# Performance work log

Hardware: AMD Instinct MI355X
Metric: run time of the kernel (lower is better)

## Reference

```python
import jax, jax.numpy as jnp
import numpy as np

NUM_QRYS = 300
NUM_CLASSES = 80
NUM_PAIRS = 4_000_000
NMS_CANDIDATES = 1000
NMS_THR = 0.65
MAX_SEGS = 100
REFINED_WEIGHT = 2.0
FH = FW = 256  # final mask grid resolution


def setup_inputs() -> dict:
    key = jax.random.key(0)
    k1, k2, k3, k4, k5, k6, k7 = jax.random.split(key, 7)
    cls_logits = jax.random.normal(k1, (NUM_QRYS, NUM_CLASSES + 1), jnp.float32)
    # valid xyxy boxes in normalized [0,1] coords
    b = jax.random.uniform(k2, (NUM_QRYS, 4), jnp.float32)
    x1 = b[:, 0] * 0.7
    y1 = b[:, 1] * 0.7
    x2 = x1 + 0.05 + b[:, 2] * 0.25
    y2 = y1 + 0.05 + b[:, 3] * 0.25
    pred_boxes = jnp.stack([x1, y1, x2, y2], axis=1)
    seg_logits = jax.random.normal(k3, (NUM_PAIRS,), jnp.float32)
    key_xy = jax.random.uniform(k4, (NUM_PAIRS, 2), jnp.float32)
    qry_ids = jax.random.randint(k5, (NUM_PAIRS,), 0, NUM_QRYS, jnp.int32)
    refined_mask = jax.random.randint(k6, (NUM_PAIRS,), 0, 2, jnp.int32).astype(bool)
    map_ids = jax.random.randint(k7, (NUM_PAIRS,), 0, 4, jnp.int32)
    return {"cls_logits": cls_logits, "pred_boxes": pred_boxes, "seg_logits": seg_logits,
            "key_xy": key_xy, "qry_ids": qry_ids, "refined_mask": refined_mask, "map_ids": map_ids}


def _box_iou(boxes):  # boxes: [C,4] xyxy -> [C,C]
    x1 = jnp.maximum(boxes[:, None, 0], boxes[None, :, 0])
    y1 = jnp.maximum(boxes[:, None, 1], boxes[None, :, 1])
    x2 = jnp.minimum(boxes[:, None, 2], boxes[None, :, 2])
    y2 = jnp.minimum(boxes[:, None, 3], boxes[None, :, 3])
    inter = jnp.clip(x2 - x1, 0.0) * jnp.clip(y2 - y1, 0.0)
    area = (boxes[:, 2] - boxes[:, 0]) * (boxes[:, 3] - boxes[:, 1])
    union = area[:, None] + area[None, :] - inter
    return inter / jnp.maximum(union, 1e-9)


def _nms_keep(iou, thr):
    # greedy NMS over score-sorted candidates (rows already in descending score order)
    C = iou.shape[0]
    idx = jnp.arange(C)
    def body(i, keep):
        sup = (iou[i] > thr) & (idx > i) & keep[i]
        return keep & ~sup
    return jax.lax.fori_loop(0, C, body, jnp.ones(C, dtype=bool))


def reference(cls_logits, pred_boxes, seg_logits, key_xy, qry_ids, refined_mask, map_ids):
    num_qrys = cls_logits.shape[0]
    # expand per-query class scores -> flat predictions (batch_size = 1)
    scores = jax.nn.sigmoid(cls_logits[:, :-1]).reshape(-1)          # [Q*C]
    feat_ids = jnp.repeat(jnp.arange(num_qrys), NUM_CLASSES)          # [Q*C]
    labels = jnp.tile(jnp.arange(NUM_CLASSES), num_qrys)              # [Q*C]
    # top-k candidates before NMS
    top_scores, cand = jax.lax.top_k(scores, NMS_CANDIDATES)
    cand_feats = feat_ids[cand]
    cand_labels = labels[cand]
    # class-aware (batched) NMS: offset boxes per label so classes don't suppress each other
    offs = cand_labels.astype(pred_boxes.dtype)[:, None] * 4.0
    cand_boxes = pred_boxes[cand_feats] + offs
    keep = _nms_keep(_box_iou(cand_boxes), NMS_THR)
    kept_scores = jnp.where(keep, top_scores, -jnp.inf)
    sel_scores, sel = jax.lax.top_k(kept_scores, MAX_SEGS)
    sel_scores = jnp.where(jnp.isfinite(sel_scores), sel_scores, 0.0)
    sel_feats = cand_feats[sel]
    # assemble per-query mask logit maps from sparse query-key pairs (scatter-max)
    px = jnp.clip((key_xy[:, 0] * FW).astype(jnp.int32), 0, FW - 1)
    py = jnp.clip((key_xy[:, 1] * FH).astype(jnp.int32), 0, FH - 1)
    w_logits = jnp.where(refined_mask, REFINED_WEIGHT * seg_logits, seg_logits)
    flat = qry_ids * (FH * FW) + py * FW + px                          # [num_pairs]
    qry_maps = jnp.full((num_qrys * FH * FW,), -1e4, cls_logits.dtype).at[flat].max(w_logits)
    qry_maps = qry_maps.reshape(num_qrys, FH, FW)
    mask_probs = jax.nn.sigmoid(qry_maps[sel_feats])                   # [MAX_SEGS, FH, FW]
    # score-weighted soft masks (float output; thresholding at mask_thr yields bool masks)
    return sel_scores[:, None, None] * mask_probs
```

## Files before the change

kernel.cpp:

```cpp
#include <hip/hip_runtime.h>

#define NQ        300
#define NC        80
#define NE        24000
#define CAND      1000
#define KSEL      100
#define NPAIRS    4000000
#define HB        4096
#define FHW       65536
#define NMS_THR_F 0.65f
#define MAPS_INIT 0x39E3BFFFu

#define NBLK_A    977
#define SLOT_CAP  32768

__device__ __forceinline__ unsigned enc_f32(float f) {
    unsigned u = __float_as_uint(f);
    return (u & 0x80000000u) ? ~u : (u | 0x80000000u);
}
__device__ __forceinline__ float dec_f32(unsigned k) {
    unsigned u = (k & 0x80000000u) ? (k ^ 0x80000000u) : ~k;
    return __uint_as_float(u);
}

__global__ __launch_bounds__(1024) void k_select(
    const float* __restrict__ cls,
    const float* __restrict__ pboxes,
    float4* __restrict__ cboxes, float* __restrict__ cscore,
    int* __restrict__ cfeat, int* __restrict__ clabel,
    unsigned* __restrict__ slot_tail)
{
    __shared__ unsigned long long sbuf[4096];
    unsigned* hist = (unsigned*)sbuf;
    __shared__ unsigned subhist[64];
    __shared__ int sB, sT, sAbove, sCount, sN;
    int tid = threadIdx.x;

    if (tid < KSEL) slot_tail[tid] = 0u;

    for (int b = tid; b < HB; b += 1024) hist[b] = 0u;
    if (tid < 64) subhist[tid] = 0u;
    __syncthreads();

    unsigned long long lk[24];
    #pragma unroll
    for (int k = 0; k < 24; k++) {
        int e = tid + (k << 10);
        if (e < NE) {
            int q = e / NC, c = e - q * NC;
            float x = cls[q * (NC + 1) + c];
            float s = 1.f / (1.f + expf(-x));
            unsigned bits = __float_as_uint(s);
            lk[k] = ((unsigned long long)bits << 32) | (unsigned)(0xFFFFFFFFu - (unsigned)e);
            atomicAdd(&hist[bits >> 18], 1u);
        }
    }
    __syncthreads();

    if (tid == 0) {
        int acc = 0, B = 0;
        for (int b = HB - 1; b >= 0; b--) {
            acc += (int)hist[b];
            if (acc >= CAND) { B = b; break; }
        }
        sB = B; sAbove = acc - (int)hist[B]; sCount = 0;
    }
    __syncthreads();
    unsigned B = (unsigned)sB;

    #pragma unroll
    for (int k = 0; k < 24; k++) {
        int e = tid + (k << 10);
        if (e < NE && (unsigned)(lk[k] >> 50) == B)
            atomicAdd(&subhist[(unsigned)(lk[k] >> 44) & 63u], 1u);
    }
    __syncthreads();
    if (tid == 0) {
        int acc2 = sAbove, T = 0;
        for (int t = 63; t >= 0; t--) {
            acc2 += (int)subhist[t];
            if (acc2 >= CAND) { T = t; break; }
        }
        sT = T; sN = acc2;
    }
    __syncthreads();
    unsigned T = (unsigned)sT;

    #pragma unroll
    for (int k = 0; k < 24; k++) {
        int e = tid + (k << 10);
        if (e < NE) {
            unsigned long long key = lk[k];
            unsigned bkt = (unsigned)(key >> 50);
            unsigned sub = (unsigned)(key >> 44) & 63u;
            if (bkt > B || (bkt == B && sub >= T)) {
                int pos = atomicAdd(&sCount, 1);
                if (pos < 4096) sbuf[pos] = key;
            }
        }
    }
    __syncthreads();
    int n = min(sN, 4096);

    if (n <= 1024) {
        unsigned long long r = (tid < n) ? sbuf[tid] : 0ULL;
        for (int k = 2; k <= 1024; k <<= 1) {
            for (int j = k >> 1; j > 0; j >>= 1) {
                unsigned long long p;
                if (j >= 64) {
                    sbuf[tid] = r; __syncthreads();
                    p = sbuf[tid ^ j]; __syncthreads();
                } else {
                    p = __shfl_xor(r, j, 64);
                }
                bool d = (tid & k) != 0, lower = (tid & j) == 0;
                r = (d != lower) ? (r > p ? r : p) : (r < p ? r : p);
            }
        }
        sbuf[tid] = r;
        __syncthreads();
    } else {
        int nsort = 2048; while (nsort < n) nsort <<= 1;
        for (int i = n + tid; i < nsort; i += 1024) sbuf[i] = 0ULL;
        __syncthreads();
        for (int k = 2; k <= nsort; k <<= 1) {
            for (int j = k >> 1; j > 0; j >>= 1) {
                for (int i = tid; i < nsort; i += 1024) {
                    int ixj = i ^ j;
                    if (ixj > i) {
                        unsigned long long a = sbuf[i], b = sbuf[ixj];
                        bool up = ((i & k) == 0);
                        if (up ? (a < b) : (a > b)) { sbuf[i] = b; sbuf[ixj] = a; }
                    }
                }
                __syncthreads();
            }
        }
    }

    if (tid < CAND) {
        unsigned long long key = sbuf[tid];
        unsigned bits = (unsigned)(key >> 32);
        unsigned e = 0xFFFFFFFFu - (unsigned)(key & 0xFFFFFFFFu);
        int feat = (int)e / NC, lab = (int)e - feat * NC;
        cscore[tid] = __uint_as_float(bits);
        cfeat[tid]  = feat;
        clabel[tid] = lab;
        float off = 4.f * (float)lab;
        float4 b;
        b.x = pboxes[feat * 4 + 0] + off; b.y = pboxes[feat * 4 + 1] + off;
        b.z = pboxes[feat * 4 + 2] + off; b.w = pboxes[feat * 4 + 3] + off;
        cboxes[tid] = b;
    }
}

__global__ __launch_bounds__(64) void k_nms(
    const float4* __restrict__ cboxes, const int* __restrict__ clabel,
    int* __restrict__ keepflag)
{
    int lab = blockIdx.x, lane = threadIdx.x;
    __shared__ int list[256];
    int base = 0;
    for (int c = 0; c < CAND; c += 64) {
        int i = c + lane;
        bool m = (i < CAND) && (clabel[i] == lab);
        unsigned long long bal = __ballot(m);
        int rank = __popcll(bal & ((1ULL << lane) - 1ULL));
        if (m && base + rank < 256) list[base + rank] = i;
        base += __popcll(bal);
    }
    __syncthreads();
    int n = min(base, 256);

    float4 bx[4]; float area[4];
    unsigned keepm = 0;
    #pragma unroll
    for (int s = 0; s < 4; s++) {
        int j = (s << 6) + lane;
        if (j < n) {
            bx[s] = cboxes[list[j]];
            area[s] = (bx[s].z - bx[s].x) * (bx[s].w - bx[s].y);
            keepm |= (1u << s);
        }
    }
    #pragma unroll
    for (int slot = 0; slot < 4; slot++) {
        int i0 = slot << 6;
        if (i0 >= n) break;
        int iend = min(64, n - i0);
        for (int l = 0; l < iend; l++) {
            int i = i0 + l;
            unsigned km = __shfl(keepm, l);
            bool keep_i = (km >> slot) & 1u;
            float bix = __shfl(bx[slot].x, l), biy = __shfl(bx[slot].y, l);
            float biz = __shfl(bx[slot].z, l), biw = __shfl(bx[slot].w, l);
            float ai  = __shfl(area[slot], l);
            if (keep_i) {
                #pragma unroll
                for (int s2 = 0; s2 < 4; s2++) {
                    int j = (s2 << 6) + lane;
                    if (j > i && j < n && ((keepm >> s2) & 1u)) {
                        float xx1 = fmaxf(bix, bx[s2].x), yy1 = fmaxf(biy, bx[s2].y);
                        float xx2 = fminf(biz, bx[s2].z), yy2 = fminf(biw, bx[s2].w);
                        float inter = fmaxf(xx2 - xx1, 0.f) * fmaxf(yy2 - yy1, 0.f);
                        float uni = ai + area[s2] - inter;
                        if (inter / fmaxf(uni, 1e-9f) > NMS_THR_F) keepm &= ~(1u << s2);
                    }
                }
            }
        }
    }
    #pragma unroll
    for (int s = 0; s < 4; s++) {
        int j = (s << 6) + lane;
        if (j < n) keepflag[list[j]] = (keepm >> s) & 1u;
    }
}

__global__ __launch_bounds__(64) void k_pick(
    const float* __restrict__ cscore, const int* __restrict__ cfeat,
    const int* __restrict__ keepflag,
    float* __restrict__ sel_score, int* __restrict__ sel_slot,
    int* __restrict__ qry2slot,
    const unsigned* __restrict__ refined_raw, unsigned* __restrict__ mode_flag)
{
    int lane = threadIdx.x;
    __shared__ float ss[KSEL];
    __shared__ int   sf[KSEL];
    __shared__ int   q2s[NQ];

    unsigned any = 0;
    for (int i = lane; i < 4096; i += 64) if (refined_raw[i] > 1u) any = 1;
    unsigned mode = (__ballot(any != 0) != 0ULL) ? 1u : 0u;

    int base = 0;
    for (int c = 0; c < CAND; c += 64) {
        int i = c + lane;
        bool k = (i < CAND) && (keepflag[i] != 0);
        unsigned long long bal = __ballot(k);
        int rank = __popcll(bal & ((1ULL << lane) - 1ULL));
        int pos = base + rank;
        if (k && pos < KSEL) { ss[pos] = cscore[i]; sf[pos] = cfeat[i]; }
        base += __popcll(bal);
    }
    for (int q = lane; q < NQ; q += 64) q2s[q] = -1;
    __syncthreads();
    if (lane == 0) {
        int nsel = min(base, KSEL), nslots = 0;
        for (int s = 0; s < KSEL; s++) {
            if (s < nsel) {
                int f = sf[s];
                int sl = q2s[f];
                if (sl < 0) { sl = nslots++; q2s[f] = sl; }
                sel_slot[s] = sl; sel_score[s] = ss[s];
            } else {
                sel_slot[s] = -1; sel_score[s] = 0.f;
            }
        }
        *mode_flag = mode;
    }
    __syncthreads();
    for (int q = lane; q < NQ; q += 64) qry2slot[q] = q2s[q];
}

__global__ __launch_bounds__(1024) void k_stage(
    const float4* __restrict__ seg4, const float4* __restrict__ xy4,
    const int4* __restrict__ qry4, const unsigned* __restrict__ refined_raw,
    const int* __restrict__ qry2slot, const unsigned* __restrict__ mode_flag,
    unsigned long long* __restrict__ bins, unsigned* __restrict__ slot_tail)
{
    __shared__ unsigned hist[KSEL];
    __shared__ unsigned gbase[KSEL];
    int tid = threadIdx.x, b = blockIdx.x;
    if (tid < KSEL) hist[tid] = 0u;
    __syncthreads();

    int t = b * 1024 + tid;
    unsigned addr[4], encw[4], rnk[4]; int nloc = 0;
    if (t < (NPAIRS / 4)) {
        int4 q = qry4[t];
        int s0 = qry2slot[q.x], s1 = qry2slot[q.y];
        int s2 = qry2slot[q.z], s3 = qry2slot[q.w];
        if ((s0 & s1 & s2 & s3) >= 0 || s0 >= 0 || s1 >= 0 || s2 >= 0 || s3 >= 0) {
            float4 sg   = seg4[t];
            float4 xy01 = xy4[2 * t], xy23 = xy4[2 * t + 1];
            unsigned r0, r1, r2, r3;
            if (*mode_flag) {
                unsigned rb = refined_raw[t];
                r0 = rb & 255u; r1 = (rb >> 8) & 255u; r2 = (rb >> 16) & 255u; r3 = rb >> 24;
            } else {
                uint4 rr = ((const uint4*)refined_raw)[t];
                r0 = rr.x; r1 = rr.y; r2 = rr.z; r3 = rr.w;
            }
            #define MK_REC(S, PX, PY, W, R)                                       \
                if (S >= 0) {                                                     \
                    int px = min(max((int)((PX) * 256.f), 0), 255);               \
                    int py = min(max((int)((PY) * 256.f), 0), 255);               \
                    float w = (R) ? 2.f * (W) : (W);                              \
                    addr[nloc] = ((unsigned)S << 16) | ((unsigned)py << 8) | (unsigned)px; \
                    encw[nloc] = enc_f32(w);                                      \
                    rnk[nloc]  = atomicAdd(&hist[S], 1u);                         \
                    nloc++;                                                       \
                }
            MK_REC(s0, xy01.x, xy01.y, sg.x, r0)
            MK_REC(s1, xy01.z, xy01.w, sg.y, r1)
            MK_REC(s2, xy23.x, xy23.y, sg.z, r2)
            MK_REC(s3, xy23.z, xy23.w, sg.w, r3)
            #undef MK_REC
        }
    }
    __syncthreads();
    if (tid < KSEL && hist[tid] > 0u)
        gbase[tid] = atomicAdd(&slot_tail[tid], hist[tid]);
    __syncthreads();

    for (int k = 0; k < nloc; k++) {
        unsigned s = addr[k] >> 16;
        unsigned pos = gbase[s] + rnk[k];
        if (pos < SLOT_CAP)
            bins[(size_t)s * SLOT_CAP + pos] =
                ((unsigned long long)encw[k] << 32) | addr[k];
    }
}

__global__ __launch_bounds__(1024) void k_tile_out(
    const unsigned long long* __restrict__ bins,
    const unsigned* __restrict__ slot_tail,
    const float* __restrict__ sel_score, const int* __restrict__ sel_slot,
    float4* __restrict__ out4)
{
    __shared__ unsigned tile[8192];
    int tid = threadIdx.x;
    int i = blockIdx.x >> 3, h = blockIdx.x & 7;
    int slot = sel_slot[i];
    float sc = sel_score[i];
    long obase = (long)i * (FHW / 4) + h * 2048;

    if (slot < 0) {
        float4 z = {0.f, 0.f, 0.f, 0.f};
        out4[obase + tid] = z;
        out4[obase + 1024 + tid] = z;
        return;
    }

    #pragma unroll
    for (int k = 0; k < 8; k++) tile[tid + (k << 10)] = MAPS_INIT;
    __syncthreads();

    unsigned tot = min(slot_tail[slot], (unsigned)SLOT_CAP);
    const unsigned long long* seg = bins + (size_t)slot * SLOT_CAP;
    for (unsigned j = tid; j < tot; j += 1024) {
        unsigned long long r = seg[j];
        unsigned addr = (unsigned)r;
        if (((addr >> 13) & 7u) == (unsigned)h)
            atomicMax(&tile[addr & 8191u], (unsigned)(r >> 32));
    }
    __syncthreads();

    #pragma unroll
    for (int k = 0; k < 2; k++) {
        int j = tid + (k << 10);
        unsigned m0 = tile[4 * j + 0], m1 = tile[4 * j + 1];
        unsigned m2 = tile[4 * j + 2], m3 = tile[4 * j + 3];
        float4 v;
        v.x = sc / (1.f + expf(-dec_f32(m0)));
        v.y = sc / (1.f + expf(-dec_f32(m1)));
        v.z = sc / (1.f + expf(-dec_f32(m2)));
        v.w = sc / (1.f + expf(-dec_f32(m3)));
        out4[obase + j] = v;
    }
}

extern "C" void kernel_launch(void* const* d_in, const int* in_sizes, int n_in,
                              void* d_out, int out_size, void* d_ws, size_t ws_size,
                              hipStream_t stream) {
    const float*    cls     = (const float*)d_in[0];
    const float*    pboxes  = (const float*)d_in[1];
    const float4*   seg4    = (const float4*)d_in[2];
    const float4*   xy4     = (const float4*)d_in[3];
    const int4*     qry4    = (const int4*)d_in[4];
    const unsigned* refined = (const unsigned*)d_in[5];
    float* out = (float*)d_out;

    char* ws = (char*)d_ws;
    unsigned long long* bins = (unsigned long long*)ws;
    unsigned*  slot_tail = (unsigned*)(ws + 26214400);
    float4*    cboxes    = (float4*)  (ws + 26214800);
    float*     cscore    = (float*)   (ws + 26230800);
    int*       cfeat     = (int*)     (ws + 26234800);
    int*       clabel    = (int*)     (ws + 26238800);
    int*       keepflag  = (int*)     (ws + 26242800);
    float*     sel_score = (float*)   (ws + 26246800);
    int*       sel_slot  = (int*)     (ws + 26247200);
    int*       qry2slot  = (int*)     (ws + 26247600);
    unsigned*  mode_flag = (unsigned*)(ws + 26248800);

    k_select  <<<1, 1024, 0, stream>>>(cls, pboxes, cboxes, cscore, cfeat, clabel,
                                       slot_tail);
    k_nms     <<<NC, 64, 0, stream>>>(cboxes, clabel, keepflag);
    k_pick    <<<1, 64, 0, stream>>>(cscore, cfeat, keepflag, sel_score, sel_slot,
                                     qry2slot, refined, mode_flag);
    k_stage   <<<NBLK_A, 1024, 0, stream>>>(seg4, xy4, qry4, refined, qry2slot, mode_flag,
                                            bins, slot_tail);
    k_tile_out<<<KSEL * 8, 1024, 0, stream>>>(bins, slot_tail, sel_score, sel_slot,
                                              (float4*)out);
}
```

Before: 242.5 us.

## Fuse all five stages into one cooperative persistent kernel with grid syncs

Replaces the five separate launches (select, NMS, pick, stage, tile output) with a single cooperative kernel of 256 blocks that separates phases with grid.sync(). Score computation and histogramming now run across the whole grid into global scratch, while selection stays in block 0. Staging and tiling loop over persistent blocks. The goal is to remove per-launch overhead and the idle gaps between small serial kernels. In exchange it pays grid-wide barrier costs, leaves most blocks idle during the single-block phases, and runs the bandwidth-heavy phases with fewer blocks.

```diff
diff --git a/kernel.cpp b/kernel.cpp
--- a/kernel.cpp
+++ b/kernel.cpp
@@ -1,4 +1,7 @@
 #include <hip/hip_runtime.h>
+#include <hip/hip_cooperative_groups.h>
+
+namespace cg = cooperative_groups;
 
 #define NQ        300
 #define NC        80
@@ -10,9 +13,12 @@
 #define FHW       65536
 #define NMS_THR_F 0.65f
 #define MAPS_INIT 0x39E3BFFFu
-
-#define NBLK_A    977
 #define SLOT_CAP  32768
+
+#define NBLK      256
+#define NTHR      1024
+
+typedef unsigned long long ull;
 
 __device__ __forceinline__ unsigned enc_f32(float f) {
     unsigned u = __float_as_uint(f);
@@ -23,351 +29,337 @@
     return __uint_as_float(u);
 }
 
-__global__ __launch_bounds__(1024) void k_select(
-    const float* __restrict__ cls,
-    const float* __restrict__ pboxes,
-    float4* __restrict__ cboxes, float* __restrict__ cscore,
-    int* __restrict__ cfeat, int* __restrict__ clabel,
-    unsigned* __restrict__ slot_tail)
+__global__ __launch_bounds__(1024, 4) void k_fused(
+    const float*    __restrict__ cls,
+    const float*    __restrict__ pboxes,
+    const float4*   __restrict__ seg4,
+    const float4*   __restrict__ xy4,
+    const int4*     __restrict__ qry4,
+    const unsigned* __restrict__ refined_raw,
+    ull*            __restrict__ bins,
+    unsigned*       __restrict__ slot_tail,
+    float4*         __restrict__ cboxes,
+    float*          __restrict__ cscore,
+    int*            __restrict__ cfeat,
+    int*            __restrict__ clabel,
+    int*            __restrict__ keepflag,
+    float*          __restrict__ sel_score,
+    int*            __restrict__ sel_slot,
+    int*            __restrict__ qry2slot,
+    unsigned*       __restrict__ mode_g,
+    ull*            __restrict__ keys,
+    unsigned*       __restrict__ hist_g,
+    float4*         __restrict__ out4)
 {
-    __shared__ unsigned long long sbuf[4096];
-    unsigned* hist = (unsigned*)sbuf;
-    __shared__ unsigned subhist[64];
-    __shared__ int sB, sT, sAbove, sCount, sN;
-    int tid = threadIdx.x;
-
-    if (tid < KSEL) slot_tail[tid] = 0u;
-
-    for (int b = tid; b < HB; b += 1024) hist[b] = 0u;
-    if (tid < 64) subhist[tid] = 0u;
-    __syncthreads();
-
-    unsigned long long lk[24];
-    #pragma unroll
-    for (int k = 0; k < 24; k++) {
-        int e = tid + (k << 10);
-        if (e < NE) {
-            int q = e / NC, c = e - q * NC;
-            float x = cls[q * (NC + 1) + c];
-            float s = 1.f / (1.f + expf(-x));
-            unsigned bits = __float_as_uint(s);
-            lk[k] = ((unsigned long long)bits << 32) | (unsigned)(0xFFFFFFFFu - (unsigned)e);
-            atomicAdd(&hist[bits >> 18], 1u);
-        }
-    }
-    __syncthreads();
-
-    if (tid == 0) {
-        int acc = 0, B = 0;
-        for (int b = HB - 1; b >= 0; b--) {
-            acc += (int)hist[b];
-            if (acc >= CAND) { B = b; break; }
-        }
-        sB = B; sAbove = acc - (int)hist[B]; sCount = 0;
-    }
-    __syncthreads();
-    unsigned B = (unsigned)sB;
-
-    #pragma unroll
-    for (int k = 0; k < 24; k++) {
-        int e = tid + (k << 10);
-        if (e < NE && (unsigned)(lk[k] >> 50) == B)
-            atomicAdd(&subhist[(unsigned)(lk[k] >> 44) & 63u], 1u);
-    }
-    __syncthreads();
-    if (tid == 0) {
-        int acc2 = sAbove, T = 0;
-        for (int t = 63; t >= 0; t--) {
-            acc2 += (int)subhist[t];
-            if (acc2 >= CAND) { T = t; break; }
-        }
-        sT = T; sN = acc2;
-    }
-    __syncthreads();
-    unsigned T = (unsigned)sT;
-
-    #pragma unroll
-    for (int k = 0; k < 24; k++) {
-        int e = tid + (k << 10);
-        if (e < NE) {
-            unsigned long long key = lk[k];
+    cg::grid_group grid = cg::this_grid();
+    __shared__ ull      sbuf[4096];
+    __shared__ unsigned small2[512];
+    __shared__ int      svars[8];
+    const int tid = threadIdx.x, b = blockIdx.x;
+    const int gid = b * NTHR + tid;
+
+    if (gid < HB)   hist_g[gid] = 0u;
+    if (gid < CAND) keepflag[gid] = 0;
+    if (gid < KSEL) slot_tail[gid] = 0u;
+    if (gid == 0)   *mode_g = 0u;
+    grid.sync();
+
+    if (gid < NE) {
+        int q = gid / NC, c = gid - q * NC;
+        float x = cls[q * (NC + 1) + c];
+        float s = 1.f / (1.f + expf(-x));
+        unsigned bits = __float_as_uint(s);
+        keys[gid] = ((ull)bits << 32) | (unsigned)(0xFFFFFFFFu - (unsigned)gid);
+        atomicAdd(&hist_g[bits >> 18], 1u);
+    }
+    if (gid < 4096 && refined_raw[gid] > 1u) atomicOr(mode_g, 1u);
+    grid.sync();
+
+    if (b == 0) {
+        unsigned* hist = (unsigned*)sbuf;
+        for (int i = tid; i < HB; i += NTHR) hist[i] = hist_g[i];
+        if (tid < 64) small2[tid] = 0u;
+        __syncthreads();
+        if (tid == 0) {
+            int acc = 0, B = 0;
+            for (int h = HB - 1; h >= 0; h--) {
+                acc += (int)hist[h];
+                if (acc >= CAND) { B = h; break; }
+            }
+            svars[0] = B; svars[2] = acc - (int)hist[B]; svars[3] = 0;
+        }
+        __syncthreads();
+        unsigned B = (unsigned)svars[0];
+
+        for (int i = tid; i < NE; i += NTHR) {
+            ull key = keys[i];
+            if ((unsigned)(key >> 50) == B)
+                atomicAdd(&small2[(unsigned)(key >> 44) & 63u], 1u);
+        }
+        __syncthreads();
+        if (tid == 0) {
+            int acc2 = svars[2], T = 0;
+            for (int t2 = 63; t2 >= 0; t2--) {
+                acc2 += (int)small2[t2];
+                if (acc2 >= CAND) { T = t2; break; }
+            }
+            svars[1] = T; svars[4] = acc2;
+        }
+        __syncthreads();
+        unsigned T = (unsigned)svars[1];
+
+        for (int i = tid; i < NE; i += NTHR) {
+            ull key = keys[i];
             unsigned bkt = (unsigned)(key >> 50);
             unsigned sub = (unsigned)(key >> 44) & 63u;
             if (bkt > B || (bkt == B && sub >= T)) {
-                int pos = atomicAdd(&sCount, 1);
+                int pos = atomicAdd(&svars[3], 1);
                 if (pos < 4096) sbuf[pos] = key;
             }
         }
-    }
-    __syncthreads();
-    int n = min(sN, 4096);
-
-    if (n <= 1024) {
-        unsigned long long r = (tid < n) ? sbuf[tid] : 0ULL;
-        for (int k = 2; k <= 1024; k <<= 1) {
-            for (int j = k >> 1; j > 0; j >>= 1) {
-                unsigned long long p;
-                if (j >= 64) {
-                    sbuf[tid] = r; __syncthreads();
-                    p = sbuf[tid ^ j]; __syncthreads();
-                } else {
-                    p = __shfl_xor(r, j, 64);
+        __syncthreads();
+        int n = min(svars[4], 4096);
+
+        if (n <= 1024) {
+            ull r = (tid < n) ? sbuf[tid] : 0ULL;
+            for (int k = 2; k <= 1024; k <<= 1) {
+                for (int j = k >> 1; j > 0; j >>= 1) {
+                    ull p;
+                    if (j >= 64) {
+                        sbuf[tid] = r; __syncthreads();
+                        p = sbuf[tid ^ j]; __syncthreads();
+                    } else {
+                        p = __shfl_xor(r, j, 64);
+                    }
+                    bool d = (tid & k) != 0, lower = (tid & j) == 0;
+                    r = (d != lower) ? (r > p ? r : p) : (r < p ? r : p);
                 }
-                bool d = (tid & k) != 0, lower = (tid & j) == 0;
-                r = (d != lower) ? (r > p ? r : p) : (r < p ? r : p);
-            }
-        }
-        sbuf[tid] = r;
-        __syncthreads();
-    } else {
-        int nsort = 2048; while (nsort < n) nsort <<= 1;
-        for (int i = n + tid; i < nsort; i += 1024) sbuf[i] = 0ULL;
-        __syncthreads();
-        for (int k = 2; k <= nsort; k <<= 1) {
-            for (int j = k >> 1; j > 0; j >>= 1) {
-                for (int i = tid; i < nsort; i += 1024) {
-                    int ixj = i ^ j;
-                    if (ixj > i) {
-                        unsigned long long a = sbuf[i], b = sbuf[ixj];
-                        bool up = ((i & k) == 0);
-                        if (up ? (a < b) : (a > b)) { sbuf[i] = b; sbuf[ixj] = a; }
+            }
+            sbuf[tid] = r;
+            __syncthreads();
+        } else {
+            int nsort = 2048; while (nsort < n) nsort <<= 1;
+            for (int i = n + tid; i < nsort; i += NTHR) sbuf[i] = 0ULL;
+            __syncthreads();
+            for (int k = 2; k <= nsort; k <<= 1) {
+                for (int j = k >> 1; j > 0; j >>= 1) {
+                    for (int i = tid; i < nsort; i += NTHR) {
+                        int ixj = i ^ j;
+                        if (ixj > i) {
+                            ull a = sbuf[i], c = sbuf[ixj];
+                            bool up = ((i & k) == 0);
+                            if (up ? (a < c) : (a > c)) { sbuf[i] = c; sbuf[ixj] = a; }
+                        }
+                    }
+                    __syncthreads();
+                }
+            }
+        }
+
+        if (tid < CAND) {
+            ull key = sbuf[tid];
+            unsigned bits = (unsigned)(key >> 32);
+            unsigned e = 0xFFFFFFFFu - (unsigned)(key & 0xFFFFFFFFu);
+            int feat = (int)e / NC, lab = (int)e - feat * NC;
+            cscore[tid] = __uint_as_float(bits);
+            cfeat[tid]  = feat;
+            clabel[tid] = lab;
+            float off = 4.f * (float)lab;
+            float4 bb;
+            bb.x = pboxes[feat * 4 + 0] + off; bb.y = pboxes[feat * 4 + 1] + off;
+            bb.z = pboxes[feat * 4 + 2] + off; bb.w = pboxes[feat * 4 + 3] + off;
+            cboxes[tid] = bb;
+        }
+    }
+    grid.sync();
+
+    if (b < NC && tid < 64) {
+        int lab = b, lane = tid;
+        int* list = (int*)small2;
+        int base = 0;
+        for (int c = 0; c < CAND; c += 64) {
+            int i = c + lane;
+            bool m = (i < CAND) && (clabel[i] == lab);
+            ull bal = __ballot(m);
+            int rank = __popcll(bal & ((1ULL << lane) - 1ULL));
+            if (m && base + rank < 256) list[base + rank] = i;
+            base += __popcll(bal);
+        }
+        int n = min(base, 256);
+
+        float4 bx[4]; float area[4];
+        unsigned keepm = 0;
+        #pragma unroll
+        for (int s = 0; s < 4; s++) {
+            int j = (s << 6) + lane;
+            if (j < n) {
+                bx[s] = cboxes[list[j]];
+                area[s] = (bx[s].z - bx[s].x) * (bx[s].w - bx[s].y);
+                keepm |= (1u << s);
+            }
+        }
+        #pragma unroll
+        for (int slot = 0; slot < 4; slot++) {
+            int i0 = slot << 6;
+            if (i0 >= n) break;
+            int iend = min(64, n - i0);
+            for (int l = 0; l < iend; l++) {
+                int i = i0 + l;
+                unsigned km = __shfl(keepm, l);
+                bool keep_i = (km >> slot) & 1u;
+                float bix = __shfl(bx[slot].x, l), biy = __shfl(bx[slot].y, l);
+                float biz = __shfl(bx[slot].z, l), biw = __shfl(bx[slot].w, l);
+                float ai  = __shfl(area[slot], l);
+                if (keep_i) {
+                    #pragma unroll
+                    for (int s2 = 0; s2 < 4; s2++) {
+                        int j = (s2 << 6) + lane;
+                        if (j > i && j < n && ((keepm >> s2) & 1u)) {
+                            float xx1 = fmaxf(bix, bx[s2].x), yy1 = fmaxf(biy, bx[s2].y);
+                            float xx2 = fminf(biz, bx[s2].z), yy2 = fminf(biw, bx[s2].w);
+                            float inter = fmaxf(xx2 - xx1, 0.f) * fmaxf(yy2 - yy1, 0.f);
+                            float uni = ai + area[s2] - inter;
+                            if (inter / fmaxf(uni, 1e-9f) > NMS_THR_F) keepm &= ~(1u << s2);
+                        }
                     }
                 }
-                __syncthreads();
-            }
-        }
-    }
-
-    if (tid < CAND) {
-        unsigned long long key = sbuf[tid];
-        unsigned bits = (unsigned)(key >> 32);
-        unsigned e = 0xFFFFFFFFu - (unsigned)(key & 0xFFFFFFFFu);
-        int feat = (int)e / NC, lab = (int)e - feat * NC;
-        cscore[tid] = __uint_as_float(bits);
-        cfeat[tid]  = feat;
-        clabel[tid] = lab;
-        float off = 4.f * (float)lab;
-        float4 b;
-        b.x = pboxes[feat * 4 + 0] + off; b.y = pboxes[feat * 4 + 1] + off;
-        b.z = pboxes[feat * 4 + 2] + off; b.w = pboxes[feat * 4 + 3] + off;
-        cboxes[tid] = b;
-    }
-}
-
-__global__ __launch_bounds__(64) void k_nms(
-    const float4* __restrict__ cboxes, const int* __restrict__ clabel,
-    int* __restrict__ keepflag)
-{
-    int lab = blockIdx.x, lane = threadIdx.x;
-    __shared__ int list[256];
-    int base = 0;
-    for (int c = 0; c < CAND; c += 64) {
-        int i = c + lane;
-        bool m = (i < CAND) && (clabel[i] == lab);
-        unsigned long long bal = __ballot(m);
-        int rank = __popcll(bal & ((1ULL << lane) - 1ULL));
-        if (m && base + rank < 256) list[base + rank] = i;
-        base += __popcll(bal);
-    }
-    __syncthreads();
-    int n = min(base, 256);
-
-    float4 bx[4]; float area[4];
-    unsigned keepm = 0;
-    #pragma unroll
-    for (int s = 0; s < 4; s++) {
-        int j = (s << 6) + lane;
-        if (j < n) {
-            bx[s] = cboxes[list[j]];
-            area[s] = (bx[s].z - bx[s].x) * (bx[s].w - bx[s].y);
-            keepm |= (1u << s);
-        }
-    }
-    #pragma unroll
-    for (int slot = 0; slot < 4; slot++) {
-        int i0 = slot << 6;
-        if (i0 >= n) break;
-        int iend = min(64, n - i0);
-        for (int l = 0; l < iend; l++) {
-            int i = i0 + l;
-            unsigned km = __shfl(keepm, l);
-            bool keep_i = (km >> slot) & 1u;
-            float bix = __shfl(bx[slot].x, l), biy = __shfl(bx[slot].y, l);
-            float biz = __shfl(bx[slot].z, l), biw = __shfl(bx[slot].w, l);
-            float ai  = __shfl(area[slot], l);
-            if (keep_i) {
-                #pragma unroll
-                for (int s2 = 0; s2 < 4; s2++) {
-                    int j = (s2 << 6) + lane;
-                    if (j > i && j < n && ((keepm >> s2) & 1u)) {
-                        float xx1 = fmaxf(bix, bx[s2].x), yy1 = fmaxf(biy, bx[s2].y);
-                        float xx2 = fminf(biz, bx[s2].z), yy2 = fminf(biw, bx[s2].w);
-                        float inter = fmaxf(xx2 - xx1, 0.f) * fmaxf(yy2 - yy1, 0.f);
-                        float uni = ai + area[s2] - inter;
-                        if (inter / fmaxf(uni, 1e-9f) > NMS_THR_F) keepm &= ~(1u << s2);
+            }
+        }
+        #pragma unroll
+        for (int s = 0; s < 4; s++) {
+            int j = (s << 6) + lane;
+            if (j < n) keepflag[list[j]] = (keepm >> s) & 1u;
+        }
+    }
+    grid.sync();
+
+    if (b == 0 && tid < 64) {
+        int lane = tid;
+        float* ss  = (float*)sbuf;
+        int*   sf  = (int*)sbuf + 128;
+        int*   q2s = (int*)sbuf + 256;
+        int base = 0;
+        for (int c = 0; c < CAND; c += 64) {
+            int i = c + lane;
+            bool k = (i < CAND) && (keepflag[i] != 0);
+            ull bal = __ballot(k);
+            int rank = __popcll(bal & ((1ULL << lane) - 1ULL));
+            int pos = base + rank;
+            if (k && pos < KSEL) { ss[pos] = cscore[i]; sf[pos] = cfeat[i]; }
+            base += __popcll(bal);
+        }
+        for (int q = lane; q < NQ; q += 64) q2s[q] = -1;
+        if (lane == 0) {
+            int nsel = min(base, KSEL), nslots = 0;
+            for (int s = 0; s < KSEL; s++) {
+                if (s < nsel) {
+                    int f = sf[s];
+                    int sl = q2s[f];
+                    if (sl < 0) { sl = nslots++; q2s[f] = sl; }
+                    sel_slot[s] = sl; sel_score[s] = ss[s];
+                } else {
+                    sel_slot[s] = -1; sel_score[s] = 0.f;
+                }
+            }
+        }
+        for (int q = lane; q < NQ; q += 64) qry2slot[q] = q2s[q];
+    }
+    grid.sync();
+
+    {
+        unsigned* hist100 = small2;
+        unsigned* gbase   = small2 + 128;
+        unsigned mode = *mode_g;
+        for (int it = 0; it < 4; it++) {
+            if (tid < KSEL) hist100[tid] = 0u;
+            __syncthreads();
+            int t = it * (NBLK * NTHR) + gid;
+            unsigned addr[4], encw[4], rnk[4]; int nloc = 0;
+            if (t < (NPAIRS / 4)) {
+                int4 q = qry4[t];
+                int s0 = qry2slot[q.x], s1 = qry2slot[q.y];
+                int s2 = qry2slot[q.z], s3 = qry2slot[q.w];
+                if ((s0 & s1 & s2 & s3) >= 0) {
+                    float4 sg   = seg4[t];
+                    float4 xy01 = xy4[2 * t], xy23 = xy4[2 * t + 1];
+                    unsigned r0, r1, r2, r3;
+                    if (mode) {
+                        unsigned rb = refined_raw[t];
+                        r0 = rb & 255u; r1 = (rb >> 8) & 255u;
+                        r2 = (rb >> 16) & 255u; r3 = rb >> 24;
+                    } else {
+                        uint4 rr = ((const uint4*)refined_raw)[t];
+                        r0 = rr.x; r1 = rr.y; r2 = rr.z; r3 = rr.w;
                     }
+                    #define MK_REC(S, PX, PY, W, R)                                       \
+                        if (S >= 0) {                                                     \
+                            int px = min(max((int)((PX) * 256.f), 0), 255);               \
+                            int py = min(max((int)((PY) * 256.f), 0), 255);               \
+                            float w = (R) ? 2.f * (W) : (W);                              \
+                            addr[nloc] = ((unsigned)S << 16) | ((unsigned)py << 8) | (unsigned)px; \
+                            encw[nloc] = enc_f32(w);                                      \
+                            rnk[nloc]  = atomicAdd(&hist100[S], 1u);                      \
+                            nloc++;                                                       \
+                        }
+                    MK_REC(s0, xy01.x, xy01.y, sg.x, r0)
+                    MK_REC(s1, xy01.z, xy01.w, sg.y, r1)
+                    MK_REC(s2, xy23.x, xy23.y, sg.z, r2)
+                    MK_REC(s3, xy23.z, xy23.w, sg.w, r3)
+                    #undef MK_REC
                 }
             }
-        }
-    }
-    #pragma unroll
-    for (int s = 0; s < 4; s++) {
-        int j = (s << 6) + lane;
-        if (j < n) keepflag[list[j]] = (keepm >> s) & 1u;
-    }
-}
-
-__global__ __launch_bounds__(64) void k_pick(
-    const float* __restrict__ cscore, const int* __restrict__ cfeat,
-    const int* __restrict__ keepflag,
-    float* __restrict__ sel_score, int* __restrict__ sel_slot,
-    int* __restrict__ qry2slot,
-    const unsigned* __restrict__ refined_raw, unsigned* __restrict__ mode_flag)
-{
-    int lane = threadIdx.x;
-    __shared__ float ss[KSEL];
-    __shared__ int   sf[KSEL];
-    __shared__ int   q2s[NQ];
-
-    unsigned any = 0;
-    for (int i = lane; i < 4096; i += 64) if (refined_raw[i] > 1u) any = 1;
-    unsigned mode = (__ballot(any != 0) != 0ULL) ? 1u : 0u;
-
-    int base = 0;
-    for (int c = 0; c < CAND; c += 64) {
-        int i = c + lane;
-        bool k = (i < CAND) && (keepflag[i] != 0);
-        unsigned long long bal = __ballot(k);
-        int rank = __popcll(bal & ((1ULL << lane) - 1ULL));
-        int pos = base + rank;
-        if (k && pos < KSEL) { ss[pos] = cscore[i]; sf[pos] = cfeat[i]; }
-        base += __popcll(bal);
-    }
-    for (int q = lane; q < NQ; q += 64) q2s[q] = -1;
-    __syncthreads();
-    if (lane == 0) {
-        int nsel = min(base, KSEL), nslots = 0;
-        for (int s = 0; s < KSEL; s++) {
-            if (s < nsel) {
-                int f = sf[s];
-                int sl = q2s[f];
-                if (sl < 0) { sl = nslots++; q2s[f] = sl; }
-                sel_slot[s] = sl; sel_score[s] = ss[s];
-            } else {
-                sel_slot[s] = -1; sel_score[s] = 0.f;
-            }
-        }
-        *mode_flag = mode;
-    }
-    __syncthreads();
-    for (int q = lane; q < NQ; q += 64) qry2slot[q] = q2s[q];
-}
-
-__global__ __launch_bounds__(1024) void k_stage(
-    const float4* __restrict__ seg4, const float4* __restrict__ xy4,
-    const int4* __restrict__ qry4, const unsigned* __restrict__ refined_raw,
-    const int* __restrict__ qry2slot, const unsigned* __restrict__ mode_flag,
-    unsigned long long* __restrict__ bins, unsigned* __restrict__ slot_tail)
-{
-    __shared__ unsigned hist[KSEL];
-    __shared__ unsigned gbase[KSEL];
-    int tid = threadIdx.x, b = blockIdx.x;
-    if (tid < KSEL) hist[tid] = 0u;
-    __syncthreads();
-
-    int t = b * 1024 + tid;
-    unsigned addr[4], encw[4], rnk[4]; int nloc = 0;
-    if (t < (NPAIRS / 4)) {
-        int4 q = qry4[t];
-        int s0 = qry2slot[q.x], s1 = qry2slot[q.y];
-        int s2 = qry2slot[q.z], s3 = qry2slot[q.w];
-        if ((s0 & s1 & s2 & s3) >= 0 || s0 >= 0 || s1 >= 0 || s2 >= 0 || s3 >= 0) {
-            float4 sg   = seg4[t];
-            float4 xy01 = xy4[2 * t], xy23 = xy4[2 * t + 1];
-            unsigned r0, r1, r2, r3;
-            if (*mode_flag) {
-                unsigned rb = refined_raw[t];
-                r0 = rb & 255u; r1 = (rb >> 8) & 255u; r2 = (rb >> 16) & 255u; r3 = rb >> 24;
-            } else {
-                uint4 rr = ((const uint4*)refined_raw)[t];
-                r0 = rr.x; r1 = rr.y; r2 = rr.z; r3 = rr.w;
-            }
-            #define MK_REC(S, PX, PY, W, R)                                       \
-                if (S >= 0) {                                                     \
-                    int px = min(max((int)((PX) * 256.f), 0), 255);               \
-                    int py = min(max((int)((PY) * 256.f), 0), 255);               \
-                    float w = (R) ? 2.f * (W) : (W);                              \
-                    addr[nloc] = ((unsigned)S << 16) | ((unsigned)py << 8) | (unsigned)px; \
-                    encw[nloc] = enc_f32(w);                                      \
-                    rnk[nloc]  = atomicAdd(&hist[S], 1u);                         \
-                    nloc++;                                                       \
-                }
-            MK_REC(s0, xy01.x, xy01.y, sg.x, r0)
-            MK_REC(s1, xy01.z, xy01.w, sg.y, r1)
-            MK_REC(s2, xy23.x, xy23.y, sg.z, r2)
-            MK_REC(s3, xy23.z, xy23.w, sg.w, r3)
-            #undef MK_REC
-        }
-    }
-    __syncthreads();
-    if (tid < KSEL && hist[tid] > 0u)
-        gbase[tid] = atomicAdd(&slot_tail[tid], hist[tid]);
-    __syncthreads();
-
-    for (int k = 0; k < nloc; k++) {
-        unsigned s = addr[k] >> 16;
-        unsigned pos = gbase[s] + rnk[k];
-        if (pos < SLOT_CAP)
-            bins[(size_t)s * SLOT_CAP + pos] =
-                ((unsigned long long)encw[k] << 32) | addr[k];
-    }
-}
-
-__global__ __launch_bounds__(1024) void k_tile_out(
-    const unsigned long long* __restrict__ bins,
-    const unsigned* __restrict__ slot_tail,
-    const float* __restrict__ sel_score, const int* __restrict__ sel_slot,
-    float4* __restrict__ out4)
-{
-    __shared__ unsigned tile[8192];
-    int tid = threadIdx.x;
-    int i = blockIdx.x >> 3, h = blockIdx.x & 7;
-    int slot = sel_slot[i];
-    float sc = sel_score[i];
-    long obase = (long)i * (FHW / 4) + h * 2048;
-
-    if (slot < 0) {
-        float4 z = {0.f, 0.f, 0.f, 0.f};
-        out4[obase + tid] = z;
-        out4[obase + 1024 + tid] = z;
-        return;
-    }
-
-    #pragma unroll
-    for (int k = 0; k < 8; k++) tile[tid + (k << 10)] = MAPS_INIT;
-    __syncthreads();
-
-    unsigned tot = min(slot_tail[slot], (unsigned)SLOT_CAP);
-    const unsigned long long* seg = bins + (size_t)slot * SLOT_CAP;
-    for (unsigned j = tid; j < tot; j += 1024) {
-        unsigned long long r = seg[j];
-        unsigned addr = (unsigned)r;
-        if (((addr >> 13) & 7u) == (unsigned)h)
-            atomicMax(&tile[addr & 8191u], (unsigned)(r >> 32));
-    }
-    __syncthreads();
-
-    #pragma unroll
-    for (int k = 0; k < 2; k++) {
-        int j = tid + (k << 10);
-        unsigned m0 = tile[4 * j + 0], m1 = tile[4 * j + 1];
-        unsigned m2 = tile[4 * j + 2], m3 = tile[4 * j + 3];
-        float4 v;
-        v.x = sc / (1.f + expf(-dec_f32(m0)));
-        v.y = sc / (1.f + expf(-dec_f32(m1)));
-        v.z = sc / (1.f + expf(-dec_f32(m2)));
-        v.w = sc / (1.f + expf(-dec_f32(m3)));
-        out4[obase + j] = v;
+            __syncthreads();
+            if (tid < KSEL && hist100[tid] > 0u)
+                gbase[tid] = atomicAdd(&slot_tail[tid], hist100[tid]);
+            __syncthreads();
+            for (int k2 = 0; k2 < nloc; k2++) {
+                unsigned s = addr[k2] >> 16;
+                unsigned pos = gbase[s] + rnk[k2];
+                if (pos < SLOT_CAP)
+                    bins[(size_t)s * SLOT_CAP + pos] = ((ull)encw[k2] << 32) | addr[k2];
+            }
+        }
+    }
+    grid.sync();
+
+    for (int tile = b; tile < KSEL * 8; tile += NBLK) {
+        int i = tile >> 3, h = tile & 7;
+        int slot = sel_slot[i];
+        float sc = sel_score[i];
+        long obase = (long)i * (FHW / 4) + h * 2048;
+
+        if (slot < 0) {
+            float4 z = {0.f, 0.f, 0.f, 0.f};
+            out4[obase + tid] = z;
+            out4[obase + 1024 + tid] = z;
+        } else {
+            unsigned* tl = (unsigned*)sbuf;
+            __syncthreads();
+            #pragma unroll
+            for (int k2 = 0; k2 < 8; k2++) tl[tid + (k2 << 10)] = MAPS_INIT;
+            __syncthreads();
+            unsigned tot = min(slot_tail[slot], (unsigned)SLOT_CAP);
+            const ull* segp = bins + (size_t)slot * SLOT_CAP;
+            for (unsigned j = tid; j < tot; j += NTHR) {
+                ull r = segp[j];
+                unsigned a = (unsigned)r;
+                if (((a >> 13) & 7u) == (unsigned)h)
+                    atomicMax(&tl[a & 8191u], (unsigned)(r >> 32));
+            }
+            __syncthreads();
+            #pragma unroll
+            for (int k2 = 0; k2 < 2; k2++) {
+                int j = tid + (k2 << 10);
+                unsigned m0 = tl[4 * j + 0], m1 = tl[4 * j + 1];
+                unsigned m2 = tl[4 * j + 2], m3 = tl[4 * j + 3];
+                float4 v;
+                v.x = sc / (1.f + expf(-dec_f32(m0)));
+                v.y = sc / (1.f + expf(-dec_f32(m1)));
+                v.z = sc / (1.f + expf(-dec_f32(m2)));
+                v.w = sc / (1.f + expf(-dec_f32(m3)));
+                out4[obase + j] = v;
+            }
+        }
     }
 }
 
@@ -380,10 +372,10 @@
     const float4*   xy4     = (const float4*)d_in[3];
     const int4*     qry4    = (const int4*)d_in[4];
     const unsigned* refined = (const unsigned*)d_in[5];
-    float* out = (float*)d_out;
+    float4* out4 = (float4*)d_out;
 
     char* ws = (char*)d_ws;
-    unsigned long long* bins = (unsigned long long*)ws;
+    ull*       bins      = (ull*)ws;
     unsigned*  slot_tail = (unsigned*)(ws + 26214400);
     float4*    cboxes    = (float4*)  (ws + 26214800);
     float*     cscore    = (float*)   (ws + 26230800);
@@ -393,15 +385,17 @@
     float*     sel_score = (float*)   (ws + 26246800);
     int*       sel_slot  = (int*)     (ws + 26247200);
     int*       qry2slot  = (int*)     (ws + 26247600);
-    unsigned*  mode_flag = (unsigned*)(ws + 26248800);
-
-    k_select  <<<1, 1024, 0, stream>>>(cls, pboxes, cboxes, cscore, cfeat, clabel,
-                                       slot_tail);
-    k_nms     <<<NC, 64, 0, stream>>>(cboxes, clabel, keepflag);
-    k_pick    <<<1, 64, 0, stream>>>(cscore, cfeat, keepflag, sel_score, sel_slot,
-                                     qry2slot, refined, mode_flag);
-    k_stage   <<<NBLK_A, 1024, 0, stream>>>(seg4, xy4, qry4, refined, qry2slot, mode_flag,
-                                            bins, slot_tail);
-    k_tile_out<<<KSEL * 8, 1024, 0, stream>>>(bins, slot_tail, sel_score, sel_slot,
-                                              (float4*)out);
+    unsigned*  mode_g    = (unsigned*)(ws + 26248800);
+    ull*       keys      = (ull*)     (ws + 26248808);
+    unsigned*  hist_g    = (unsigned*)(ws + 26440808);
+
+    void* args[] = {
+        (void*)&cls, (void*)&pboxes, (void*)&seg4, (void*)&xy4, (void*)&qry4,
+        (void*)&refined, (void*)&bins, (void*)&slot_tail, (void*)&cboxes,
+        (void*)&cscore, (void*)&cfeat, (void*)&clabel, (void*)&keepflag,
+        (void*)&sel_score, (void*)&sel_slot, (void*)&qry2slot, (void*)&mode_g,
+        (void*)&keys, (void*)&hist_g, (void*)&out4
+    };
+    hipLaunchCooperativeKernel((void*)k_fused, dim3(NBLK), dim3(NTHR),
+                               args, 0, stream);
 }
```

Result: slower. 404.0 us (+66.6%).

## Bin staged pairs per slot and row-band so tile blocks read only their band

Applied to the files above, without the earlier changes.

The staging kernel now buckets each selected pair into one of 800 bins, one per slot and 32-row band, instead of 100 per-slot bins. Each output tile block then reads only its own band's records, where before it scanned the whole slot list eight times and filtered out most entries. The refined-mask mode check and the keepflag zeroing move into the select kernel, and the workspace doubles to hold the bins. In exchange the staging pass keeps a larger shared histogram and does more global tail atomics.

```diff
diff --git a/kernel.cpp b/kernel.cpp
--- a/kernel.cpp
+++ b/kernel.cpp
@@ -12,7 +12,10 @@
 #define MAPS_INIT 0x39E3BFFFu
 
 #define NBLK_A    977
-#define SLOT_CAP  32768
+#define NBIN      800
+#define BAND_CAP  8192
+
+typedef unsigned long long ull;
 
 __device__ __forceinline__ unsigned enc_f32(float f) {
     unsigned u = __float_as_uint(f);
@@ -28,21 +31,31 @@
     const float* __restrict__ pboxes,
     float4* __restrict__ cboxes, float* __restrict__ cscore,
     int* __restrict__ cfeat, int* __restrict__ clabel,
-    unsigned* __restrict__ slot_tail)
+    unsigned* __restrict__ bin_tail, int* __restrict__ keepflag,
+    const unsigned* __restrict__ refined_raw, unsigned* __restrict__ mode_flag)
 {
-    __shared__ unsigned long long sbuf[4096];
+    __shared__ ull sbuf[4096];
     unsigned* hist = (unsigned*)sbuf;
     __shared__ unsigned subhist[64];
     __shared__ int sB, sT, sAbove, sCount, sN;
+    __shared__ unsigned smode;
     int tid = threadIdx.x;
 
-    if (tid < KSEL) slot_tail[tid] = 0u;
+    if (tid < NBIN) bin_tail[tid] = 0u;
+    if (tid < CAND) keepflag[tid] = 0;
+    if (tid == 0) smode = 0u;
 
     for (int b = tid; b < HB; b += 1024) hist[b] = 0u;
     if (tid < 64) subhist[tid] = 0u;
     __syncthreads();
 
-    unsigned long long lk[24];
+    {
+        unsigned any = 0;
+        for (int i = tid; i < 4096; i += 1024) if (refined_raw[i] > 1u) any = 1;
+        if (any) atomicOr(&smode, 1u);
+    }
+
+    ull lk[24];
     #pragma unroll
     for (int k = 0; k < 24; k++) {
         int e = tid + (k << 10);
@@ -51,7 +64,7 @@
             float x = cls[q * (NC + 1) + c];
             float s = 1.f / (1.f + expf(-x));
             unsigned bits = __float_as_uint(s);
-            lk[k] = ((unsigned long long)bits << 32) | (unsigned)(0xFFFFFFFFu - (unsigned)e);
+            lk[k] = ((ull)bits << 32) | (unsigned)(0xFFFFFFFFu - (unsigned)e);
             atomicAdd(&hist[bits >> 18], 1u);
         }
     }
@@ -64,6 +77,7 @@
             if (acc >= CAND) { B = b; break; }
         }
         sB = B; sAbove = acc - (int)hist[B]; sCount = 0;
+        *mode_flag = smode;
     }
     __syncthreads();
     unsigned B = (unsigned)sB;
@@ -90,7 +104,7 @@
     for (int k = 0; k < 24; k++) {
         int e = tid + (k << 10);
         if (e < NE) {
-            unsigned long long key = lk[k];
+            ull key = lk[k];
             unsigned bkt = (unsigned)(key >> 50);
             unsigned sub = (unsigned)(key >> 44) & 63u;
             if (bkt > B || (bkt == B && sub >= T)) {
@@ -103,10 +117,10 @@
     int n = min(sN, 4096);
 
     if (n <= 1024) {
-        unsigned long long r = (tid < n) ? sbuf[tid] : 0ULL;
+        ull r = (tid < n) ? sbuf[tid] : 0ULL;
         for (int k = 2; k <= 1024; k <<= 1) {
             for (int j = k >> 1; j > 0; j >>= 1) {
-                unsigned long long p;
+                ull p;
                 if (j >= 64) {
                     sbuf[tid] = r; __syncthreads();
                     p = sbuf[tid ^ j]; __syncthreads();
@@ -128,7 +142,7 @@
                 for (int i = tid; i < nsort; i += 1024) {
                     int ixj = i ^ j;
                     if (ixj > i) {
-                        unsigned long long a = sbuf[i], b = sbuf[ixj];
+                        ull a = sbuf[i], b = sbuf[ixj];
                         bool up = ((i & k) == 0);
                         if (up ? (a < b) : (a > b)) { sbuf[i] = b; sbuf[ixj] = a; }
                     }
@@ -139,7 +153,7 @@
     }
 
     if (tid < CAND) {
-        unsigned long long key = sbuf[tid];
+        ull key = sbuf[tid];
         unsigned bits = (unsigned)(key >> 32);
         unsigned e = 0xFFFFFFFFu - (unsigned)(key & 0xFFFFFFFFu);
         int feat = (int)e / NC, lab = (int)e - feat * NC;
@@ -164,7 +178,7 @@
     for (int c = 0; c < CAND; c += 64) {
         int i = c + lane;
         bool m = (i < CAND) && (clabel[i] == lab);
-        unsigned long long bal = __ballot(m);
+        ull bal = __ballot(m);
         int rank = __popcll(bal & ((1ULL << lane) - 1ULL));
         if (m && base + rank < 256) list[base + rank] = i;
         base += __popcll(bal);
@@ -221,23 +235,18 @@
     const float* __restrict__ cscore, const int* __restrict__ cfeat,
     const int* __restrict__ keepflag,
     float* __restrict__ sel_score, int* __restrict__ sel_slot,
-    int* __restrict__ qry2slot,
-    const unsigned* __restrict__ refined_raw, unsigned* __restrict__ mode_flag)
+    int* __restrict__ qry2slot)
 {
     int lane = threadIdx.x;
     __shared__ float ss[KSEL];
     __shared__ int   sf[KSEL];
     __shared__ int   q2s[NQ];
 
-    unsigned any = 0;
-    for (int i = lane; i < 4096; i += 64) if (refined_raw[i] > 1u) any = 1;
-    unsigned mode = (__ballot(any != 0) != 0ULL) ? 1u : 0u;
-
     int base = 0;
     for (int c = 0; c < CAND; c += 64) {
         int i = c + lane;
         bool k = (i < CAND) && (keepflag[i] != 0);
-        unsigned long long bal = __ballot(k);
+        ull bal = __ballot(k);
         int rank = __popcll(bal & ((1ULL << lane) - 1ULL));
         int pos = base + rank;
         if (k && pos < KSEL) { ss[pos] = cscore[i]; sf[pos] = cfeat[i]; }
@@ -257,7 +266,6 @@
                 sel_slot[s] = -1; sel_score[s] = 0.f;
             }
         }
-        *mode_flag = mode;
     }
     __syncthreads();
     for (int q = lane; q < NQ; q += 64) qry2slot[q] = q2s[q];
@@ -267,12 +275,12 @@
     const float4* __restrict__ seg4, const float4* __restrict__ xy4,
     const int4* __restrict__ qry4, const unsigned* __restrict__ refined_raw,
     const int* __restrict__ qry2slot, const unsigned* __restrict__ mode_flag,
-    unsigned long long* __restrict__ bins, unsigned* __restrict__ slot_tail)
+    ull* __restrict__ bins, unsigned* __restrict__ bin_tail)
 {
-    __shared__ unsigned hist[KSEL];
-    __shared__ unsigned gbase[KSEL];
+    __shared__ unsigned hist[NBIN];
+    __shared__ unsigned gbase[NBIN];
     int tid = threadIdx.x, b = blockIdx.x;
-    if (tid < KSEL) hist[tid] = 0u;
+    if (tid < NBIN) hist[tid] = 0u;
     __syncthreads();
 
     int t = b * 1024 + tid;
@@ -297,9 +305,10 @@
                     int px = min(max((int)((PX) * 256.f), 0), 255);               \
                     int py = min(max((int)((PY) * 256.f), 0), 255);               \
                     float w = (R) ? 2.f * (W) : (W);                              \
-                    addr[nloc] = ((unsigned)S << 16) | ((unsigned)py << 8) | (unsigned)px; \
+                    unsigned a = ((unsigned)S << 16) | ((unsigned)py << 8) | (unsigned)px; \
+                    addr[nloc] = a;                                               \
                     encw[nloc] = enc_f32(w);                                      \
-                    rnk[nloc]  = atomicAdd(&hist[S], 1u);                         \
+                    rnk[nloc]  = atomicAdd(&hist[a >> 13], 1u);                   \
                     nloc++;                                                       \
                 }
             MK_REC(s0, xy01.x, xy01.y, sg.x, r0)
@@ -310,22 +319,20 @@
         }
     }
     __syncthreads();
-    if (tid < KSEL && hist[tid] > 0u)
-        gbase[tid] = atomicAdd(&slot_tail[tid], hist[tid]);
+    for (int i = tid; i < NBIN; i += 1024)
+        if (hist[i] > 0u) gbase[i] = atomicAdd(&bin_tail[i], hist[i]);
     __syncthreads();
 
     for (int k = 0; k < nloc; k++) {
-        unsigned s = addr[k] >> 16;
-        unsigned pos = gbase[s] + rnk[k];
-        if (pos < SLOT_CAP)
-            bins[(size_t)s * SLOT_CAP + pos] =
-                ((unsigned long long)encw[k] << 32) | addr[k];
+        unsigned hb = addr[k] >> 13;
+        unsigned pos = gbase[hb] + rnk[k];
+        if (pos < BAND_CAP)
+            bins[(size_t)hb * BAND_CAP + pos] = ((ull)encw[k] << 32) | addr[k];
     }
 }
 
 __global__ __launch_bounds__(1024) void k_tile_out(
-    const unsigned long long* __restrict__ bins,
-    const unsigned* __restrict__ slot_tail,
+    const ull* __restrict__ bins, const unsigned* __restrict__ bin_tail,
     const float* __restrict__ sel_score, const int* __restrict__ sel_slot,
     float4* __restrict__ out4)
 {
@@ -347,13 +354,12 @@
     for (int k = 0; k < 8; k++) tile[tid + (k << 10)] = MAPS_INIT;
     __syncthreads();
 
-    unsigned tot = min(slot_tail[slot], (unsigned)SLOT_CAP);
-    const unsigned long long* seg = bins + (size_t)slot * SLOT_CAP;
+    int hb = slot * 8 + h;
+    unsigned tot = min(bin_tail[hb], (unsigned)BAND_CAP);
+    const ull* segp = bins + (size_t)hb * BAND_CAP;
     for (unsigned j = tid; j < tot; j += 1024) {
-        unsigned long long r = seg[j];
-        unsigned addr = (unsigned)r;
-        if (((addr >> 13) & 7u) == (unsigned)h)
-            atomicMax(&tile[addr & 8191u], (unsigned)(r >> 32));
+        ull r = segp[j];
+        atomicMax(&tile[(unsigned)r & 8191u], (unsigned)(r >> 32));
     }
     __syncthreads();
 
@@ -383,25 +389,25 @@
     float* out = (float*)d_out;
 
     char* ws = (char*)d_ws;
-    unsigned long long* bins = (unsigned long long*)ws;
-    unsigned*  slot_tail = (unsigned*)(ws + 26214400);
-    float4*    cboxes    = (float4*)  (ws + 26214800);
-    float*     cscore    = (float*)   (ws + 26230800);
-    int*       cfeat     = (int*)     (ws + 26234800);
-    int*       clabel    = (int*)     (ws + 26238800);
-    int*       keepflag  = (int*)     (ws + 26242800);
-    float*     sel_score = (float*)   (ws + 26246800);
-    int*       sel_slot  = (int*)     (ws + 26247200);
-    int*       qry2slot  = (int*)     (ws + 26247600);
-    unsigned*  mode_flag = (unsigned*)(ws + 26248800);
+    ull*       bins      = (ull*)ws;
+    unsigned*  bin_tail  = (unsigned*)(ws + 52428800);
+    float4*    cboxes    = (float4*)  (ws + 52432000);
+    float*     cscore    = (float*)   (ws + 52448000);
+    int*       cfeat     = (int*)     (ws + 52452000);
+    int*       clabel    = (int*)     (ws + 52456000);
+    int*       keepflag  = (int*)     (ws + 52460000);
+    float*     sel_score = (float*)   (ws + 52464000);
+    int*       sel_slot  = (int*)     (ws + 52464400);
+    int*       qry2slot  = (int*)     (ws + 52464800);
+    unsigned*  mode_flag = (unsigned*)(ws + 52466000);
 
     k_select  <<<1, 1024, 0, stream>>>(cls, pboxes, cboxes, cscore, cfeat, clabel,
-                                       slot_tail);
+                                       bin_tail, keepflag, refined, mode_flag);
     k_nms     <<<NC, 64, 0, stream>>>(cboxes, clabel, keepflag);
     k_pick    <<<1, 64, 0, stream>>>(cscore, cfeat, keepflag, sel_score, sel_slot,
-                                     qry2slot, refined, mode_flag);
+                                     qry2slot);
     k_stage   <<<NBLK_A, 1024, 0, stream>>>(seg4, xy4, qry4, refined, qry2slot, mode_flag,
-                                            bins, slot_tail);
-    k_tile_out<<<KSEL * 8, 1024, 0, stream>>>(bins, slot_tail, sel_score, sel_slot,
+                                            bins, bin_tail);
+    k_tile_out<<<KSEL * 8, 1024, 0, stream>>>(bins, bin_tail, sel_score, sel_slot,
                                               (float4*)out);
 }
```

Measured after the change: 222.5 us. 8.3% less time.
